# Performance work log

Hardware: AMD Instinct MI355X
Metric: run time of the kernel (lower is better)

The kernel has to match this reference:

```python
import jax, jax.numpy as jnp
import numpy as np

PATCH_SIZE = 16
HOP_DISTANCE = 7.0


def setup_inputs() -> dict:
    key = jax.random.key(0)
    x = jax.random.normal(key, (1, 1024, 1024), dtype=jnp.float32)
    return {"x": x}


def _patchify(x, p):
    # Faithful replication of F.unfold(kernel=p, stride=p) followed by .view(-1, p, p)
    # on the contiguous [1, C*p*p, L] unfold output (row-major reshape).
    C, H, W = x.shape
    nH, nW = H // p, W // p
    # unfold layout: [C*p*p, L] with element (c*p*p + ki*p + kj, bi*nW + bj)
    cols = x.reshape(C, nH, p, nW, p).transpose(0, 2, 4, 1, 3).reshape(C * p * p, nH * nW)
    # torch .view(-1, p, p) on contiguous [C*p*p, L] == row-major reshape
    return cols.reshape(-1, p, p)  # [N, p, p], N = C * nH * nW


def reference(x):
    p = PATCH_SIZE
    patches = _patchify(x, p)  # [N, p, p]
    # distance(patch_i, patch_j) = norm over dim=1 (rows) -> per-column vector of length p.
    # d2[i, j, k] = sum_r (patches[i, r, k] - patches[j, r, k])**2, via Gram trick.
    sq = jnp.sum(patches * patches, axis=1)                      # [N, p]
    G = jnp.einsum('irk,jrk->ijk', patches, patches)             # [N, N, p]
    d2 = jnp.maximum(sq[:, None, :] + sq[None, :, :] - 2.0 * G, 0.0)
    # A[i, j] = 1 iff all per-column norms <= hop_distance
    A = jnp.all(jnp.sqrt(d2) <= HOP_DISTANCE, axis=-1).astype(jnp.float32)  # [N, N]
    return A
```

## Files before the change

kernel.cpp:

```cpp
#include <hip/hip_runtime.h>


#define NPATCH 4096
#define BT 64
#define KC 2
#define NPH 8

__global__ __launch_bounds__(256, 3) void adj_kernel(const float* __restrict__ x,
                                                     float* __restrict__ A) {
#pragma clang fp contract(off)
    __shared__ float4 Si[BT][8];
    __shared__ float4 Sj[BT][8];
    __shared__ float sqs[2][KC][BT];

    int t = blockIdx.x;
    int bi = (int)((sqrtf(8.0f * (float)t + 1.0f) - 1.0f) * 0.5f);
    while ((bi + 1) * (bi + 2) / 2 <= t) ++bi;
    while (bi * (bi + 1) / 2 > t) --bi;
    int bj = t - bi * (bi + 1) / 2;

    const int i0 = bi * BT;
    const int j0 = bj * BT;
    const int tid = threadIdx.x;
    const int tx = tid & 15;
    const int ty = tid >> 4;

    float m[4][4];
#pragma unroll
    for (int u = 0; u < 4; ++u)
#pragma unroll
        for (int v = 0; v < 4; ++v) m[u][v] = -3.0e38f;

    for (int kp = 0; kp < NPH; ++kp) {
        __syncthreads();
#pragma unroll
        for (int l = 0; l < 4; ++l) {
            int gid = l * 256 + tid;
            int side = gid >> 9;
            int q = gid & 511;
            int kl = q & 1;
            int r = (q >> 1) & 15;
            int rl = q >> 5;
            int k = kp * KC + kl;
            int b = side ? bj : bi;
            int h = rl * 64 + (r >> 2) * 16 + (b >> 2);
            int w0 = (r & 3) * 256 + k * 16 + ((4 * b) & 15);
            float4 v = *(const float4*)&x[h * 1024 + w0];
            const float* vp = (const float*)&v;
            int c = (kl << 2) | (r >> 2);
            int e = r & 3;
            float4* Sb = side ? &Sj[0][0] : &Si[0][0];
#pragma unroll
            for (int dd = 0; dd < 4; ++dd) {
                int row = 16 * dd + rl;
                int ch = c ^ ((row >> 2) & 7);
                ((float*)&Sb[row * 8 + ch])[e] = vp[dd];
            }
        }
        __syncthreads();
        {
            int side = tid >> 7;
            int kl = (tid >> 6) & 1;
            int row = tid & 63;
            const float4* Sb = side ? &Sj[row][0] : &Si[row][0];
            int swz = (row >> 2) & 7;
            float acc;
            {
                float4 v = Sb[(kl * 4) ^ swz];
                acc = v.x * v.x;
                float t1 = v.y * v.y; acc = acc + t1;
                float t2 = v.z * v.z; acc = acc + t2;
                float t3 = v.w * v.w; acc = acc + t3;
            }
#pragma unroll
            for (int rc = 1; rc < 4; ++rc) {
                float4 v = Sb[(kl * 4 + rc) ^ swz];
                float t0 = v.x * v.x; acc = acc + t0;
                float t1 = v.y * v.y; acc = acc + t1;
                float t2 = v.z * v.z; acc = acc + t2;
                float t3 = v.w * v.w; acc = acc + t3;
            }
            sqs[side][kl][row] = acc;
        }
        __syncthreads();
#pragma unroll
        for (int kl = 0; kl < KC; ++kl) {
            float d[4][4];
#pragma unroll
            for (int u = 0; u < 4; ++u)
#pragma unroll
                for (int v = 0; v < 4; ++v) d[u][v] = 0.0f;
#pragma unroll
            for (int rc = 0; rc < 4; ++rc) {
                int c = kl * 4 + rc;
                float4 a[4], b[4];
#pragma unroll
                for (int u = 0; u < 4; ++u)
                    a[u] = Si[ty * 4 + u][c ^ (ty & 7)];
#pragma unroll
                for (int v = 0; v < 4; ++v)
                    b[v] = Sj[tx * 4 + v][c ^ (tx & 7)];
#pragma unroll
                for (int u = 0; u < 4; ++u)
#pragma unroll
                    for (int v = 0; v < 4; ++v) {
                        d[u][v] = fmaf(a[u].x, b[v].x, d[u][v]);
                        d[u][v] = fmaf(a[u].y, b[v].y, d[u][v]);
                        d[u][v] = fmaf(a[u].z, b[v].z, d[u][v]);
                        d[u][v] = fmaf(a[u].w, b[v].w, d[u][v]);
                    }
            }
            float4 si4 = *(const float4*)&sqs[0][kl][ty * 4];
            float4 sj4 = *(const float4*)&sqs[1][kl][tx * 4];
            const float* sip = (const float*)&si4;
            const float* sjp = (const float*)&sj4;
#pragma unroll
            for (int u = 0; u < 4; ++u)
#pragma unroll
                for (int v = 0; v < 4; ++v) {
                    float s = sip[u] + sjp[v];
                    float d2 = fmaf(-2.0f, d[u][v], s);
                    m[u][v] = fmaxf(m[u][v], d2);
                }
        }
    }

#pragma unroll
    for (int u = 0; u < 4; ++u) {
        float4 o;
        o.x = (m[u][0] <= 49.0f) ? 1.0f : 0.0f;
        o.y = (m[u][1] <= 49.0f) ? 1.0f : 0.0f;
        o.z = (m[u][2] <= 49.0f) ? 1.0f : 0.0f;
        o.w = (m[u][3] <= 49.0f) ? 1.0f : 0.0f;
        *(float4*)&A[(size_t)(i0 + ty * 4 + u) * NPATCH + j0 + tx * 4] = o;
    }
    if (bi != bj) {
#pragma unroll
        for (int v = 0; v < 4; ++v) {
            float4 o;
            o.x = (m[0][v] <= 49.0f) ? 1.0f : 0.0f;
            o.y = (m[1][v] <= 49.0f) ? 1.0f : 0.0f;
            o.z = (m[2][v] <= 49.0f) ? 1.0f : 0.0f;
            o.w = (m[3][v] <= 49.0f) ? 1.0f : 0.0f;
            *(float4*)&A[(size_t)(j0 + tx * 4 + v) * NPATCH + i0 + ty * 4] = o;
        }
    }
}

extern "C" void kernel_launch(void* const* d_in, const int* in_sizes, int n_in,
                              void* d_out, int out_size, void* d_ws, size_t ws_size,
                              hipStream_t stream) {
    const float* x = (const float*)d_in[0];
    float* A = (float*)d_out;
    (void)d_ws; (void)ws_size;

    const int nblk = (NPATCH / BT) * (NPATCH / BT + 1) / 2;
    adj_kernel<<<nblk, 256, 0, stream>>>(x, A);
}
```

Before: 157.8 us.

## Halve block threads with 8x4 micro-tiles and bitmask threshold accumulation

Block size drops from 256 to 128 threads, so each thread now computes an 8x4 micro-tile of the 64x64 output tile instead of 4x4, which raises register-level reuse of the shared-memory operand loads. The 16 running max accumulators are replaced by one 32-bit mask that records any column exceeding the threshold, which frees registers for the larger tile. The loading and squared-norm loops are adjusted to cover the same data with fewer threads. The cost is less parallelism per block and more registers per thread, and the launch bounds change to (128, 2).

After: 185.2 us. 1.17x slower.

```diff
diff --git a/kernel.cpp b/kernel.cpp
--- a/kernel.cpp
+++ b/kernel.cpp
@@ -6,7 +6,7 @@
 #define KC 2
 #define NPH 8
 
-__global__ __launch_bounds__(256, 3) void adj_kernel(const float* __restrict__ x,
+__global__ __launch_bounds__(128, 2) void adj_kernel(const float* __restrict__ x,
                                                      float* __restrict__ A) {
 #pragma clang fp contract(off)
     __shared__ float4 Si[BT][8];
@@ -25,17 +25,13 @@
     const int tx = tid & 15;
     const int ty = tid >> 4;
 
-    float m[4][4];
-#pragma unroll
-    for (int u = 0; u < 4; ++u)
-#pragma unroll
-        for (int v = 0; v < 4; ++v) m[u][v] = -3.0e38f;
+    unsigned int bad = 0u;
 
     for (int kp = 0; kp < NPH; ++kp) {
         __syncthreads();
 #pragma unroll
-        for (int l = 0; l < 4; ++l) {
-            int gid = l * 256 + tid;
+        for (int l = 0; l < 8; ++l) {
+            int gid = l * 128 + tid;
             int side = gid >> 9;
             int q = gid & 511;
             int kl = q & 1;
@@ -58,10 +54,12 @@
             }
         }
         __syncthreads();
-        {
-            int side = tid >> 7;
-            int kl = (tid >> 6) & 1;
-            int row = tid & 63;
+#pragma unroll
+        for (int p = 0; p < 2; ++p) {
+            int s0 = p * 128 + tid;
+            int side = s0 >> 7;
+            int kl = (s0 >> 6) & 1;
+            int row = s0 & 63;
             const float4* Sb = side ? &Sj[row][0] : &Si[row][0];
             int swz = (row >> 2) & 7;
             float acc;
@@ -85,23 +83,23 @@
         __syncthreads();
 #pragma unroll
         for (int kl = 0; kl < KC; ++kl) {
-            float d[4][4];
+            float d[8][4];
 #pragma unroll
-            for (int u = 0; u < 4; ++u)
+            for (int u = 0; u < 8; ++u)
 #pragma unroll
                 for (int v = 0; v < 4; ++v) d[u][v] = 0.0f;
 #pragma unroll
             for (int rc = 0; rc < 4; ++rc) {
                 int c = kl * 4 + rc;
-                float4 a[4], b[4];
+                float4 a[8], b[4];
 #pragma unroll
-                for (int u = 0; u < 4; ++u)
-                    a[u] = Si[ty * 4 + u][c ^ (ty & 7)];
+                for (int u = 0; u < 8; ++u)
+                    a[u] = Si[ty * 8 + u][c ^ ((2 * ty + (u >> 2)) & 7)];
 #pragma unroll
                 for (int v = 0; v < 4; ++v)
                     b[v] = Sj[tx * 4 + v][c ^ (tx & 7)];
 #pragma unroll
-                for (int u = 0; u < 4; ++u)
+                for (int u = 0; u < 8; ++u)
 #pragma unroll
                     for (int v = 0; v < 4; ++v) {
                         d[u][v] = fmaf(a[u].x, b[v].x, d[u][v]);
@@ -110,39 +108,41 @@
                         d[u][v] = fmaf(a[u].w, b[v].w, d[u][v]);
                     }
             }
-            float4 si4 = *(const float4*)&sqs[0][kl][ty * 4];
-            float4 sj4 = *(const float4*)&sqs[1][kl][tx * 4];
-            const float* sip = (const float*)&si4;
-            const float* sjp = (const float*)&sj4;
 #pragma unroll
-            for (int u = 0; u < 4; ++u)
+            for (int u = 0; u < 8; ++u) {
+                float si = sqs[0][kl][ty * 8 + u];
 #pragma unroll
                 for (int v = 0; v < 4; ++v) {
-                    float s = sip[u] + sjp[v];
+                    float sj = sqs[1][kl][tx * 4 + v];
+                    float s = si + sj;
                     float d2 = fmaf(-2.0f, d[u][v], s);
-                    m[u][v] = fmaxf(m[u][v], d2);
+                    bad |= (d2 > 49.0f) ? (1u << (u * 4 + v)) : 0u;
                 }
+            }
         }
     }
 
 #pragma unroll
-    for (int u = 0; u < 4; ++u) {
+    for (int u = 0; u < 8; ++u) {
         float4 o;
-        o.x = (m[u][0] <= 49.0f) ? 1.0f : 0.0f;
-        o.y = (m[u][1] <= 49.0f) ? 1.0f : 0.0f;
-        o.z = (m[u][2] <= 49.0f) ? 1.0f : 0.0f;
-        o.w = (m[u][3] <= 49.0f) ? 1.0f : 0.0f;
-        *(float4*)&A[(size_t)(i0 + ty * 4 + u) * NPATCH + j0 + tx * 4] = o;
+        o.x = (bad >> (u * 4 + 0)) & 1u ? 0.0f : 1.0f;
+        o.y = (bad >> (u * 4 + 1)) & 1u ? 0.0f : 1.0f;
+        o.z = (bad >> (u * 4 + 2)) & 1u ? 0.0f : 1.0f;
+        o.w = (bad >> (u * 4 + 3)) & 1u ? 0.0f : 1.0f;
+        *(float4*)&A[(size_t)(i0 + ty * 8 + u) * NPATCH + j0 + tx * 4] = o;
     }
     if (bi != bj) {
 #pragma unroll
         for (int v = 0; v < 4; ++v) {
-            float4 o;
-            o.x = (m[0][v] <= 49.0f) ? 1.0f : 0.0f;
-            o.y = (m[1][v] <= 49.0f) ? 1.0f : 0.0f;
-            o.z = (m[2][v] <= 49.0f) ? 1.0f : 0.0f;
-            o.w = (m[3][v] <= 49.0f) ? 1.0f : 0.0f;
-            *(float4*)&A[(size_t)(j0 + tx * 4 + v) * NPATCH + i0 + ty * 4] = o;
+#pragma unroll
+            for (int g = 0; g < 2; ++g) {
+                float4 o;
+                o.x = (bad >> ((g * 4 + 0) * 4 + v)) & 1u ? 0.0f : 1.0f;
+                o.y = (bad >> ((g * 4 + 1) * 4 + v)) & 1u ? 0.0f : 1.0f;
+                o.z = (bad >> ((g * 4 + 2) * 4 + v)) & 1u ? 0.0f : 1.0f;
+                o.w = (bad >> ((g * 4 + 3) * 4 + v)) & 1u ? 0.0f : 1.0f;
+                *(float4*)&A[(size_t)(j0 + tx * 4 + v) * NPATCH + i0 + ty * 8 + g * 4] = o;
+            }
         }
     }
 }
@@ -155,5 +155,5 @@
     (void)d_ws; (void)ws_size;
 
     const int nblk = (NPATCH / BT) * (NPATCH / BT + 1) / 2;
-    adj_kernel<<<nblk, 256, 0, stream>>>(x, A);
+    adj_kernel<<<nblk, 128, 0, stream>>>(x, A);
 }
```

## Transpose shared tiles to pair columns and use packed FP32 FMA

Applied to the files above, without the earlier changes.

Shared-memory tiles are re-laid out row-major by patch row, with the two column channels of each patch packed side by side and padded and swizzled against bank conflicts. The inner product loop then runs v_pk_fma_f32 through inline assembly, so one instruction updates both column distances. The running max per pair is replaced by a 16-bit mask of threshold violations, which frees registers. The squared-norm pass now uses only half the threads, and the packed layout and inline asm add complexity and depend on the compiler scheduling around the asm.

Result: slower. 161.8 us (+2.5%).

```diff
diff --git a/kernel.cpp b/kernel.cpp
--- a/kernel.cpp
+++ b/kernel.cpp
@@ -3,15 +3,20 @@
 
 #define NPATCH 4096
 #define BT 64
-#define KC 2
 #define NPH 8
+#define CH 33
+
+typedef float v2f __attribute__((ext_vector_type(2)));
+typedef float v4f __attribute__((ext_vector_type(4)));
+
+__device__ __forceinline__ int fsw(int i) { return i ^ (i >> 3); }
 
 __global__ __launch_bounds__(256, 3) void adj_kernel(const float* __restrict__ x,
                                                      float* __restrict__ A) {
 #pragma clang fp contract(off)
-    __shared__ float4 Si[BT][8];
-    __shared__ float4 Sj[BT][8];
-    __shared__ float sqs[2][KC][BT];
+    __shared__ v4f SiT[16 * CH];
+    __shared__ v4f SjT[16 * CH];
+    __shared__ float sqs[2][2][BT];
 
     int t = blockIdx.x;
     int bi = (int)((sqrtf(8.0f * (float)t + 1.0f) - 1.0f) * 0.5f);
@@ -24,12 +29,10 @@
     const int tid = threadIdx.x;
     const int tx = tid & 15;
     const int ty = tid >> 4;
+    const int cA0 = fsw(ty * 2), cA1 = fsw(ty * 2 + 1);
+    const int cB0 = fsw(tx * 2), cB1 = fsw(tx * 2 + 1);
 
-    float m[4][4];
-#pragma unroll
-    for (int u = 0; u < 4; ++u)
-#pragma unroll
-        for (int v = 0; v < 4; ++v) m[u][v] = -3.0e38f;
+    unsigned int bad = 0u;
 
     for (int kp = 0; kp < NPH; ++kp) {
         __syncthreads();
@@ -41,107 +44,98 @@
             int kl = q & 1;
             int r = (q >> 1) & 15;
             int rl = q >> 5;
-            int k = kp * KC + kl;
+            int k = kp * 2 + kl;
             int b = side ? bj : bi;
             int h = rl * 64 + (r >> 2) * 16 + (b >> 2);
             int w0 = (r & 3) * 256 + k * 16 + ((4 * b) & 15);
             float4 v = *(const float4*)&x[h * 1024 + w0];
             const float* vp = (const float*)&v;
-            int c = (kl << 2) | (r >> 2);
-            int e = r & 3;
-            float4* Sb = side ? &Sj[0][0] : &Si[0][0];
+            float* Sb = side ? (float*)SjT : (float*)SiT;
+            int slot = (rl & 1) * 2 + kl;
 #pragma unroll
             for (int dd = 0; dd < 4; ++dd) {
-                int row = 16 * dd + rl;
-                int ch = c ^ ((row >> 2) & 7);
-                ((float*)&Sb[row * 8 + ch])[e] = vp[dd];
+                int rowpair = 8 * dd + (rl >> 1);
+                Sb[(r * CH + fsw(rowpair)) * 4 + slot] = vp[dd];
             }
         }
         __syncthreads();
-        {
-            int side = tid >> 7;
-            int kl = (tid >> 6) & 1;
+        if (tid < 128) {
+            int side = tid >> 6;
             int row = tid & 63;
-            const float4* Sb = side ? &Sj[row][0] : &Si[row][0];
-            int swz = (row >> 2) & 7;
-            float acc;
+            const v4f* Sb = side ? SjT : SiT;
+            int rp = fsw(row >> 1);
+            int s0 = (row & 1) * 2;
+            float acc0, acc1;
             {
-                float4 v = Sb[(kl * 4) ^ swz];
-                acc = v.x * v.x;
-                float t1 = v.y * v.y; acc = acc + t1;
-                float t2 = v.z * v.z; acc = acc + t2;
-                float t3 = v.w * v.w; acc = acc + t3;
+                v4f v = Sb[rp];
+                float e0 = v[s0], e1 = v[s0 + 1];
+                acc0 = e0 * e0;
+                acc1 = e1 * e1;
             }
 #pragma unroll
-            for (int rc = 1; rc < 4; ++rc) {
-                float4 v = Sb[(kl * 4 + rc) ^ swz];
-                float t0 = v.x * v.x; acc = acc + t0;
-                float t1 = v.y * v.y; acc = acc + t1;
-                float t2 = v.z * v.z; acc = acc + t2;
-                float t3 = v.w * v.w; acc = acc + t3;
+            for (int r = 1; r < 16; ++r) {
+                v4f v = Sb[r * CH + rp];
+                float e0 = v[s0], e1 = v[s0 + 1];
+                float t0 = e0 * e0; acc0 = acc0 + t0;
+                float t1 = e1 * e1; acc1 = acc1 + t1;
             }
-            sqs[side][kl][row] = acc;
+            sqs[side][0][row] = acc0;
+            sqs[side][1][row] = acc1;
         }
         __syncthreads();
+        v2f d[4][4];
 #pragma unroll
-        for (int kl = 0; kl < KC; ++kl) {
-            float d[4][4];
+        for (int u = 0; u < 4; ++u)
+#pragma unroll
+            for (int v = 0; v < 4; ++v) d[u][v] = (v2f)(0.0f);
+#pragma unroll
+        for (int r = 0; r < 16; ++r) {
+            v4f a0 = SiT[r * CH + cA0];
+            v4f a1 = SiT[r * CH + cA1];
+            v4f b0 = SjT[r * CH + cB0];
+            v4f b1 = SjT[r * CH + cB1];
+            v2f ap[4] = { a0.xy, a0.zw, a1.xy, a1.zw };
+            v2f bp[4] = { b0.xy, b0.zw, b1.xy, b1.zw };
 #pragma unroll
             for (int u = 0; u < 4; ++u)
 #pragma unroll
-                for (int v = 0; v < 4; ++v) d[u][v] = 0.0f;
+                for (int v = 0; v < 4; ++v)
+                    asm("v_pk_fma_f32 %0, %1, %2, %0"
+                        : "+v"(d[u][v]) : "v"(ap[u]), "v"(bp[v]));
+        }
+        v4f si0 = *(const v4f*)&sqs[0][0][ty * 4];
+        v4f si1 = *(const v4f*)&sqs[0][1][ty * 4];
+        v4f sj0 = *(const v4f*)&sqs[1][0][tx * 4];
+        v4f sj1 = *(const v4f*)&sqs[1][1][tx * 4];
 #pragma unroll
-            for (int rc = 0; rc < 4; ++rc) {
-                int c = kl * 4 + rc;
-                float4 a[4], b[4];
+        for (int u = 0; u < 4; ++u)
 #pragma unroll
-                for (int u = 0; u < 4; ++u)
-                    a[u] = Si[ty * 4 + u][c ^ (ty & 7)];
-#pragma unroll
-                for (int v = 0; v < 4; ++v)
-                    b[v] = Sj[tx * 4 + v][c ^ (tx & 7)];
-#pragma unroll
-                for (int u = 0; u < 4; ++u)
-#pragma unroll
-                    for (int v = 0; v < 4; ++v) {
-                        d[u][v] = fmaf(a[u].x, b[v].x, d[u][v]);
-                        d[u][v] = fmaf(a[u].y, b[v].y, d[u][v]);
-                        d[u][v] = fmaf(a[u].z, b[v].z, d[u][v]);
-                        d[u][v] = fmaf(a[u].w, b[v].w, d[u][v]);
-                    }
+            for (int v = 0; v < 4; ++v) {
+                float s0 = si0[u] + sj0[v];
+                float s1 = si1[u] + sj1[v];
+                float d20 = fmaf(-2.0f, d[u][v].x, s0);
+                float d21 = fmaf(-2.0f, d[u][v].y, s1);
+                bad |= ((d20 > 49.0f) || (d21 > 49.0f)) ? (1u << (u * 4 + v)) : 0u;
             }
-            float4 si4 = *(const float4*)&sqs[0][kl][ty * 4];
-            float4 sj4 = *(const float4*)&sqs[1][kl][tx * 4];
-            const float* sip = (const float*)&si4;
-            const float* sjp = (const float*)&sj4;
-#pragma unroll
-            for (int u = 0; u < 4; ++u)
-#pragma unroll
-                for (int v = 0; v < 4; ++v) {
-                    float s = sip[u] + sjp[v];
-                    float d2 = fmaf(-2.0f, d[u][v], s);
-                    m[u][v] = fmaxf(m[u][v], d2);
-                }
-        }
     }
 
 #pragma unroll
     for (int u = 0; u < 4; ++u) {
         float4 o;
-        o.x = (m[u][0] <= 49.0f) ? 1.0f : 0.0f;
-        o.y = (m[u][1] <= 49.0f) ? 1.0f : 0.0f;
-        o.z = (m[u][2] <= 49.0f) ? 1.0f : 0.0f;
-        o.w = (m[u][3] <= 49.0f) ? 1.0f : 0.0f;
+        o.x = (bad >> (u * 4 + 0)) & 1u ? 0.0f : 1.0f;
+        o.y = (bad >> (u * 4 + 1)) & 1u ? 0.0f : 1.0f;
+        o.z = (bad >> (u * 4 + 2)) & 1u ? 0.0f : 1.0f;
+        o.w = (bad >> (u * 4 + 3)) & 1u ? 0.0f : 1.0f;
         *(float4*)&A[(size_t)(i0 + ty * 4 + u) * NPATCH + j0 + tx * 4] = o;
     }
     if (bi != bj) {
 #pragma unroll
         for (int v = 0; v < 4; ++v) {
             float4 o;
-            o.x = (m[0][v] <= 49.0f) ? 1.0f : 0.0f;
-            o.y = (m[1][v] <= 49.0f) ? 1.0f : 0.0f;
-            o.z = (m[2][v] <= 49.0f) ? 1.0f : 0.0f;
-            o.w = (m[3][v] <= 49.0f) ? 1.0f : 0.0f;
+            o.x = (bad >> (0 * 4 + v)) & 1u ? 0.0f : 1.0f;
+            o.y = (bad >> (1 * 4 + v)) & 1u ? 0.0f : 1.0f;
+            o.z = (bad >> (2 * 4 + v)) & 1u ? 0.0f : 1.0f;
+            o.w = (bad >> (3 * 4 + v)) & 1u ? 0.0f : 1.0f;
             *(float4*)&A[(size_t)(j0 + tx * 4 + v) * NPATCH + i0 + ty * 4] = o;
         }
     }
```
